# Performance work log

Measured on AMD Instinct MI355X. Metric: run time of the kernel, lower is better.

## Reference

```python
import jax, jax.numpy as jnp
import numpy as np

B, V = 256, 128000

def setup_inputs() -> dict:
    key = jax.random.key(0)
    k1, k2 = jax.random.split(key)
    logits = jax.random.normal(k1, (B, V), dtype=jnp.float32)
    # temperatures in [0.5, 1.5) to avoid degenerate near-zero temps
    temperatures = jax.random.uniform(k2, (B,), dtype=jnp.float32, minval=0.5, maxval=1.5)
    return {"logits": logits, "temperatures": temperatures, "top_k": 50}

def reference(logits, temperatures, top_k):
    # temperature scale (logits.float().div_(temps[:, None]))
    scaled = logits.astype(jnp.float32) / temperatures[:, None]          # [B, V]
    # top-k threshold: k-th largest value per row
    kth = jax.lax.top_k(scaled, top_k)[0][:, -1:]                        # [B, 1]
    # mask everything strictly below the k-th value to -inf
    masked = jnp.where(scaled < kth, -jnp.inf, scaled)                   # [B, V]
    # softmax + multinomial(1)  ==  categorical over masked logits
    samples = jax.random.categorical(jax.random.key(42), masked, axis=-1)  # [B]
    return samples
```

## Files before the change

kernel.cpp:

```cpp
#include <hip/hip_runtime.h>

#define T1 256
#define SPLIT 8
#define LDSCAP 1024
#define OVF_MARK 0xFFFFFFFFu

#define T2 1024
#define BINS 4096
#define CAPF 4096
#define FLOOR_KEY 0xC0200000u
#define FLOOR_BITS 0x40200000u
#define FLOOR_RANGE 0x3FE00000u
#define MARGIN 8u

__device__ __forceinline__ unsigned rotl32(unsigned x, unsigned r) {
  return (x << r) | (x >> (32u - r));
}

__device__ __forceinline__ unsigned threefry_xor_0_42(unsigned x0, unsigned x1) {
  const unsigned k0 = 0u, k1 = 42u, k2 = 0u ^ 42u ^ 0x1BD11BDAu;
  x0 += k0; x1 += k1;
#define TF_R(r) { x0 += x1; x1 = rotl32(x1, r); x1 ^= x0; }
  TF_R(13) TF_R(15) TF_R(26) TF_R(6)
  x0 += k1; x1 += k2 + 1u;
  TF_R(17) TF_R(29) TF_R(16) TF_R(24)
  x0 += k2; x1 += k0 + 2u;
  TF_R(13) TF_R(15) TF_R(26) TF_R(6)
  x0 += k0; x1 += k1 + 3u;
  TF_R(17) TF_R(29) TF_R(16) TF_R(24)
  x0 += k1; x1 += k2 + 4u;
  TF_R(13) TF_R(15) TF_R(26) TF_R(6)
  x0 += k2; x1 += k0 + 5u;
#undef TF_R
  return x0 ^ x1;
}

__device__ __forceinline__ float gumbel_at(unsigned flat) {
  unsigned bits = threefry_xor_0_42(0u, flat);
  float fl = __uint_as_float((bits >> 9) | 0x3F800000u) - 1.0f;
  const float tiny = 1.17549435e-38f;
  float u = fmaxf(fl + tiny, tiny);
  return -logf(-logf(u));
}

__device__ __forceinline__ unsigned f2k(float f) {
  unsigned b = __float_as_uint(f);
  return (b & 0x80000000u) ? ~b : (b ^ 0x80000000u);
}
__device__ __forceinline__ float k2f(unsigned k) {
  unsigned b = (k & 0x80000000u) ? (k ^ 0x80000000u) : ~k;
  return __uint_as_float(b);
}

__global__ __launch_bounds__(T1, 8) void scan_kernel(
    const float* __restrict__ logits, unsigned* __restrict__ counts,
    unsigned* __restrict__ okeys, unsigned* __restrict__ oidxs, int V) {
  const int row = blockIdx.x >> 3;
  const int chunk = blockIdx.x & (SPLIT - 1);
  const int tid = threadIdx.x;
  const int nv4 = V >> 2;
  const int c4 = (nv4 + SPLIT - 1) / SPLIT;
  const int beg = chunk * c4;
  const int end = min(nv4, beg + c4);
  const float* rowp = logits + (size_t)row * (size_t)V;
  const float4* rowp4 = (const float4*)rowp;

  __shared__ unsigned skey[LDSCAP];
  __shared__ unsigned sidx[LDSCAP];
  __shared__ unsigned snc;
  if (tid == 0) snc = 0u;
  __syncthreads();

#define TEST1(vv, col) do {                                              \
    unsigned b_ = __float_as_uint(vv);                                   \
    if (__builtin_expect(b_ - FLOOR_BITS < FLOOR_RANGE, 0)) {            \
      unsigned p_ = atomicAdd(&snc, 1u);                                 \
      if (p_ < LDSCAP) { skey[p_] = b_ ^ 0x80000000u; sidx[p_] = (unsigned)(col); } \
    } } while (0)
#define TEST4(vv, i4) do {                                               \
    TEST1((vv).x, (i4) * 4 + 0); TEST1((vv).y, (i4) * 4 + 1);            \
    TEST1((vv).z, (i4) * 4 + 2); TEST1((vv).w, (i4) * 4 + 3); } while (0)

  int i = beg + tid;
  for (; i + 3 * T1 < end; i += 4 * T1) {
    float4 v0 = rowp4[i];
    float4 v1 = rowp4[i + T1];
    float4 v2 = rowp4[i + 2 * T1];
    float4 v3 = rowp4[i + 3 * T1];
    TEST4(v0, i); TEST4(v1, i + T1); TEST4(v2, i + 2 * T1); TEST4(v3, i + 3 * T1);
  }
  for (; i < end; i += T1) { float4 v = rowp4[i]; TEST4(v, i); }
  if (chunk == SPLIT - 1) {
    for (int j = nv4 * 4 + tid; j < V; j += T1) TEST1(rowp[j], j);
  }
#undef TEST4
#undef TEST1
  __syncthreads();

  const unsigned nc = snc;
  const unsigned nb = min(nc, (unsigned)LDSCAP);
  if (tid == 0) counts[row * SPLIT + chunk] = (nc > (unsigned)LDSCAP) ? OVF_MARK : nc;
  unsigned* kout = okeys + (size_t)(row * SPLIT + chunk) * LDSCAP;
  unsigned* iout = oidxs + (size_t)(row * SPLIT + chunk) * LDSCAP;
  for (unsigned p = tid; p < nb; p += T1) { kout[p] = skey[p]; iout[p] = sidx[p]; }
}

__global__ __launch_bounds__(T2) void select_kernel(
    const float* __restrict__ logits, const float* __restrict__ temps,
    const int* __restrict__ topk_ptr, const unsigned* __restrict__ counts,
    const unsigned* __restrict__ okeys, const unsigned* __restrict__ oidxs,
    int* __restrict__ out, int V) {
  const int row = blockIdx.x;
  const int tid = threadIdx.x;
  const unsigned K = (unsigned)(*topk_ptr);
  const float t = temps[row];
  const unsigned rowBase = (unsigned)row * (unsigned)V;
  const float* rowp = logits + (size_t)row * (size_t)V;
  const float4* rowp4 = (const float4*)rowp;
  const int nv4 = V >> 2;

  __shared__ unsigned hist[BINS];
  __shared__ unsigned cand_key[CAPF];
  __shared__ unsigned cand_idx[CAPF];
  __shared__ float    rv[T2];
  __shared__ unsigned ri[T2];
  __shared__ unsigned soff[SPLIT + 1];
  __shared__ int      sovf;
  __shared__ unsigned ncand, sBstar, sAbove, sK50;

  if (tid == 0) {
    ncand = 0u; sBstar = 0u; sAbove = 0u; sK50 = 0u;
    unsigned s = 0; int ovf = 0;
    const unsigned* c8 = counts + row * SPLIT;
#pragma unroll
    for (int cch = 0; cch < SPLIT; ++cch) {
      unsigned n = c8[cch];
      if (n == OVF_MARK) { ovf = 1; n = 0u; }
      soff[cch] = s; s += n;
    }
    soff[SPLIT] = s; sovf = ovf;
  }
  __syncthreads();

  const unsigned total = soff[SPLIT];
  const bool tryFast = (!sovf && total >= K && total <= (unsigned)CAPF);
  unsigned c = 0;
  unsigned cntAbove = 0;

  if (tryFast) {
    c = total;
#pragma unroll
    for (int cch = 0; cch < SPLIT; ++cch) {
      const unsigned off = soff[cch];
      const unsigned nbc = soff[cch + 1] - off;
      const unsigned* kin = okeys + (size_t)(row * SPLIT + cch) * LDSCAP;
      const unsigned* iin = oidxs + (size_t)(row * SPLIT + cch) * LDSCAP;
      for (unsigned p = tid; p < nbc; p += T2) {
        cand_key[off + p] = kin[p];
        cand_idx[off + p] = iin[p];
      }
    }
    __syncthreads();
    for (unsigned i = tid; i < c; i += T2) {
      unsigned ki = cand_key[i];
      unsigned gt = 0, eq = 0;
      for (unsigned j = 0; j < c; ++j) {
        unsigned kj = cand_key[j];
        gt += (kj > ki) ? 1u : 0u;
        eq += (kj == ki) ? 1u : 0u;
      }
      if (gt < K && gt + eq >= K) sK50 = ki;
    }
    __syncthreads();
  }

  const bool fastOK = tryFast && (sK50 >= FLOOR_KEY + MARGIN);

  float bestV = -INFINITY;
  unsigned bestI = 0xFFFFFFFFu;

  if (!fastOK) {
    for (int i = tid; i < BINS; i += T2) hist[i] = 0u;
    if (tid == 0) { ncand = 0u; sK50 = 0u; }
    __syncthreads();

    for (int i = tid; i < nv4; i += T2) {
      float4 v = rowp4[i];
      atomicAdd(&hist[f2k(v.x) >> 20], 1u);
      atomicAdd(&hist[f2k(v.y) >> 20], 1u);
      atomicAdd(&hist[f2k(v.z) >> 20], 1u);
      atomicAdd(&hist[f2k(v.w) >> 20], 1u);
    }
    for (int j = nv4 * 4 + tid; j < V; j += T2) atomicAdd(&hist[f2k(rowp[j]) >> 20], 1u);
    __syncthreads();

    if (tid < 64) {
      const int lane = tid;
      unsigned s = 0;
      for (int k = 0; k < 64; ++k) s += hist[lane * 64 + k];
      unsigned suf = s;
#pragma unroll
      for (int off = 1; off < 64; off <<= 1) {
        unsigned o = __shfl_down(suf, off);
        if (lane + off < 64) suf += o;
      }
      unsigned sufn = __shfl_down(suf, 1);
      if (lane == 63) sufn = 0u;
      if (suf >= K && sufn < K) {
        unsigned run = sufn;
        for (int k = 63; k >= 0; --k) {
          unsigned h = hist[lane * 64 + k];
          unsigned nr = run + h;
          if (run < K && nr >= K) { sBstar = (unsigned)(lane * 64 + k); sAbove = run; }
          run = nr;
        }
      }
    }
    __syncthreads();

    const unsigned Bstar = sBstar;
    cntAbove = sAbove;
    const unsigned long long binCeilP1 = ((unsigned long long)(Bstar + 1u)) << 20;
    const unsigned lowKey = (Bstar >= 1u) ? ((Bstar - 1u) << 20) : 0u;

    for (int i = tid; i < nv4; i += T2) {
      float4 v = rowp4[i];
      float f[4] = {v.x, v.y, v.z, v.w};
#pragma unroll
      for (int e = 0; e < 4; ++e) {
        unsigned key = f2k(f[e]);
        if (key < lowKey) continue;
        unsigned col = (unsigned)(i * 4 + e);
        if ((unsigned long long)key >= binCeilP1) {
          float sj = f[e] / t;
          float val = sj + gumbel_at(rowBase + col);
          if (val > bestV || (val == bestV && col < bestI)) { bestV = val; bestI = col; }
        } else {
          unsigned p = atomicAdd(&ncand, 1u);
          if (p < CAPF) { cand_key[p] = key; cand_idx[p] = col; }
        }
      }
    }
    for (int j = nv4 * 4 + tid; j < V; j += T2) {
      unsigned key = f2k(rowp[j]);
      if (key < lowKey) continue;
      if ((unsigned long long)key >= binCeilP1) {
        float sj = rowp[j] / t;
        float val = sj + gumbel_at(rowBase + (unsigned)j);
        if (val > bestV || (val == bestV && (unsigned)j < bestI)) { bestV = val; bestI = (unsigned)j; }
      } else {
        unsigned p = atomicAdd(&ncand, 1u);
        if (p < CAPF) { cand_key[p] = key; cand_idx[p] = (unsigned)j; }
      }
    }
    __syncthreads();

    c = min(ncand, (unsigned)CAPF);
    for (unsigned i = tid; i < c; i += T2) {
      unsigned ki = cand_key[i];
      unsigned gt = 0, eq = 0;
      for (unsigned j = 0; j < c; ++j) {
        unsigned kj = cand_key[j];
        gt += (kj > ki) ? 1u : 0u;
        eq += (kj == ki) ? 1u : 0u;
      }
      if (cntAbove + gt < K && cntAbove + gt + eq >= K) sK50 = ki;
    }
    __syncthreads();
  }

  const float s50 = k2f(sK50) / t;
  for (unsigned i = tid; i < c; i += T2) {
    unsigned col = cand_idx[i];
    if (col >= (unsigned)V) continue;
    float sj = k2f(cand_key[i]) / t;
    if (sj >= s50) {
      float val = sj + gumbel_at(rowBase + col);
      if (val > bestV || (val == bestV && col < bestI)) { bestV = val; bestI = col; }
    }
  }

  rv[tid] = bestV; ri[tid] = bestI;
  __syncthreads();
  for (int off = T2 / 2; off > 0; off >>= 1) {
    if (tid < off) {
      float v2 = rv[tid + off]; unsigned i2 = ri[tid + off];
      if (v2 > rv[tid] || (v2 == rv[tid] && i2 < ri[tid])) { rv[tid] = v2; ri[tid] = i2; }
    }
    __syncthreads();
  }
  if (tid == 0) out[row] = (int)((ri[0] < (unsigned)V) ? ri[0] : 0u);
}

extern "C" void kernel_launch(void* const* d_in, const int* in_sizes, int n_in,
                              void* d_out, int out_size, void* d_ws, size_t ws_size,
                              hipStream_t stream) {
  const float* logits = (const float*)d_in[0];
  const float* temps  = (const float*)d_in[1];
  const int*   topk   = (const int*)d_in[2];
  int* out = (int*)d_out;

  const int B = in_sizes[1];
  const int V = in_sizes[0] / B;

  unsigned* counts = (unsigned*)d_ws;
  unsigned* okeys = counts + (size_t)B * SPLIT;
  unsigned* oidxs = okeys + (size_t)B * SPLIT * LDSCAP;

  scan_kernel<<<B * SPLIT, T1, 0, stream>>>(logits, counts, okeys, oidxs, V);
  select_kernel<<<B, T2, 0, stream>>>(logits, temps, topk, counts, okeys, oidxs, out, V);
}
```

Measured before the change: 228.2 us.

## Deepen scan loads to 8 strided float4s and aggregate LDS atomics per wavefront

Measured after the change: 227.1 us. No clear change (-0.5%).

```diff
diff --git a/kernel.cpp b/kernel.cpp
--- a/kernel.cpp
+++ b/kernel.cpp
@@ -2,6 +2,7 @@
 
 #define T1 256
 #define SPLIT 8
+#define DEPTH 8
 #define LDSCAP 1024
 #define OVF_MARK 0xFFFFFFFFu
 
@@ -52,16 +53,17 @@
   return __uint_as_float(b);
 }
 
-__global__ __launch_bounds__(T1, 8) void scan_kernel(
+__global__ __launch_bounds__(T1, 4) void scan_kernel(
     const float* __restrict__ logits, unsigned* __restrict__ counts,
     unsigned* __restrict__ okeys, unsigned* __restrict__ oidxs, int V) {
   const int row = blockIdx.x >> 3;
   const int chunk = blockIdx.x & (SPLIT - 1);
   const int tid = threadIdx.x;
+  const int lane = tid & 63;
   const int nv4 = V >> 2;
-  const int c4 = (nv4 + SPLIT - 1) / SPLIT;
+  const int c4 = nv4 / SPLIT;
   const int beg = chunk * c4;
-  const int end = min(nv4, beg + c4);
+  const int sub = c4 / DEPTH;
   const float* rowp = logits + (size_t)row * (size_t)V;
   const float4* rowp4 = (const float4*)rowp;
 
@@ -71,30 +73,48 @@
   if (tid == 0) snc = 0u;
   __syncthreads();
 
-#define TEST1(vv, col) do {                                              \
-    unsigned b_ = __float_as_uint(vv);                                   \
-    if (__builtin_expect(b_ - FLOOR_BITS < FLOOR_RANGE, 0)) {            \
-      unsigned p_ = atomicAdd(&snc, 1u);                                 \
-      if (p_ < LDSCAP) { skey[p_] = b_ ^ 0x80000000u; sidx[p_] = (unsigned)(col); } \
+#define PROC1(fv, col) do {                                                  \
+    unsigned b_ = __float_as_uint(fv);                                       \
+    bool p_ = (b_ - FLOOR_BITS) < FLOOR_RANGE;                               \
+    unsigned long long m_ = __ballot(p_);                                    \
+    if (m_) {                                                                \
+      int lead_ = __builtin_ctzll(m_);                                       \
+      unsigned base_ = 0u;                                                   \
+      if (lane == lead_) base_ = atomicAdd(&snc, (unsigned)__popcll(m_));    \
+      base_ = __shfl(base_, lead_);                                          \
+      if (p_) {                                                              \
+        unsigned my_ = base_ + (unsigned)__popcll(m_ & ((1ull << lane) - 1ull)); \
+        if (my_ < LDSCAP) { skey[my_] = b_ ^ 0x80000000u; sidx[my_] = (unsigned)(col); } \
+      }                                                                      \
     } } while (0)
-#define TEST4(vv, i4) do {                                               \
-    TEST1((vv).x, (i4) * 4 + 0); TEST1((vv).y, (i4) * 4 + 1);            \
-    TEST1((vv).z, (i4) * 4 + 2); TEST1((vv).w, (i4) * 4 + 3); } while (0)
-
-  int i = beg + tid;
-  for (; i + 3 * T1 < end; i += 4 * T1) {
-    float4 v0 = rowp4[i];
-    float4 v1 = rowp4[i + T1];
-    float4 v2 = rowp4[i + 2 * T1];
-    float4 v3 = rowp4[i + 3 * T1];
-    TEST4(v0, i); TEST4(v1, i + T1); TEST4(v2, i + 2 * T1); TEST4(v3, i + 3 * T1);
-  }
-  for (; i < end; i += T1) { float4 v = rowp4[i]; TEST4(v, i); }
+#define PROC4(vv, i4) do {                                                   \
+    PROC1((vv).x, (i4) * 4 + 0); PROC1((vv).y, (i4) * 4 + 1);                \
+    PROC1((vv).z, (i4) * 4 + 2); PROC1((vv).w, (i4) * 4 + 3); } while (0)
+
+  for (int off = tid; off < sub; off += T1) {
+    const int i0 = beg + off;
+    float4 v0 = rowp4[i0 + 0 * sub];
+    float4 v1 = rowp4[i0 + 1 * sub];
+    float4 v2 = rowp4[i0 + 2 * sub];
+    float4 v3 = rowp4[i0 + 3 * sub];
+    float4 v4 = rowp4[i0 + 4 * sub];
+    float4 v5 = rowp4[i0 + 5 * sub];
+    float4 v6 = rowp4[i0 + 6 * sub];
+    float4 v7 = rowp4[i0 + 7 * sub];
+    PROC4(v0, i0 + 0 * sub); PROC4(v1, i0 + 1 * sub);
+    PROC4(v2, i0 + 2 * sub); PROC4(v3, i0 + 3 * sub);
+    PROC4(v4, i0 + 4 * sub); PROC4(v5, i0 + 5 * sub);
+    PROC4(v6, i0 + 6 * sub); PROC4(v7, i0 + 7 * sub);
+  }
+  for (int i = beg + DEPTH * sub + tid; i < beg + c4; i += T1) {
+    float4 v = rowp4[i]; PROC4(v, i);
+  }
   if (chunk == SPLIT - 1) {
-    for (int j = nv4 * 4 + tid; j < V; j += T1) TEST1(rowp[j], j);
-  }
-#undef TEST4
-#undef TEST1
+    for (int i = SPLIT * c4 + tid; i < nv4; i += T1) { float4 v = rowp4[i]; PROC4(v, i); }
+    for (int j = nv4 * 4 + tid; j < V; j += T1) PROC1(rowp[j], j);
+  }
+#undef PROC4
+#undef PROC1
   __syncthreads();
 
   const unsigned nc = snc;
```
